# Kernel optimization log

Measured on AMD Instinct MI355X. Metric: run time of the kernel, lower is better.

Reference implementation:

```python
import jax, jax.numpy as jnp
import numpy as np
from functools import partial

INPUT_SIZE = 24
HIDDEN = 64
NUM_LAYERS = 3
OUT_FEATURES = 4


def _lstm_layer(x, w_ih, w_hh, b_ih, b_hh):
    """Single LSTM layer, PyTorch gate order (i, f, g, o).
    x: [B, T, in] -> returns h sequence [B, T, H]."""
    B = x.shape[0]
    H = w_hh.shape[1]
    # Precompute input contribution for all timesteps: [B, T, 4H]
    gx = jnp.einsum('bti,gi->btg', x, w_ih) + b_ih + b_hh

    def step(carry, g_t):
        h, c = carry
        gates = g_t + h @ w_hh.T  # [B, 4H]
        i, f, g, o = jnp.split(gates, 4, axis=-1)
        i = jax.nn.sigmoid(i)
        f = jax.nn.sigmoid(f)
        g = jnp.tanh(g)
        o = jax.nn.sigmoid(o)
        c = f * c + i * g
        h = o * jnp.tanh(c)
        return (h, c), h

    h0 = jnp.zeros((B, H), dtype=x.dtype)
    c0 = jnp.zeros((B, H), dtype=x.dtype)
    (_, _), hs = jax.lax.scan(step, (h0, c0), jnp.swapaxes(gx, 0, 1))  # hs: [T, B, H]
    return jnp.swapaxes(hs, 0, 1)  # [B, T, H]


def setup_inputs() -> dict:
    key = jax.random.key(0)
    ks = jax.random.split(key, 16)
    B, T = 1024, 512
    inp = {"x": jax.random.normal(ks[0], (B, T, INPUT_SIZE), dtype=jnp.float32)}
    k = 1
    s = 1.0 / np.sqrt(HIDDEN)
    for layer in range(NUM_LAYERS):
        in_dim = INPUT_SIZE if layer == 0 else HIDDEN
        inp[f"w_ih_{layer}"] = jax.random.uniform(ks[k], (4 * HIDDEN, in_dim), minval=-s, maxval=s, dtype=jnp.float32); k += 1
        inp[f"w_hh_{layer}"] = jax.random.uniform(ks[k], (4 * HIDDEN, HIDDEN), minval=-s, maxval=s, dtype=jnp.float32); k += 1
        inp[f"b_ih_{layer}"] = jax.random.uniform(ks[k], (4 * HIDDEN,), minval=-s, maxval=s, dtype=jnp.float32); k += 1
        inp[f"b_hh_{layer}"] = jax.random.uniform(ks[k], (4 * HIDDEN,), minval=-s, maxval=s, dtype=jnp.float32); k += 1
    inp["w_lin"] = jax.random.uniform(ks[13], (OUT_FEATURES, HIDDEN), minval=-s, maxval=s, dtype=jnp.float32)
    inp["b_lin"] = jax.random.uniform(ks[14], (OUT_FEATURES,), minval=-s, maxval=s, dtype=jnp.float32)
    return inp


def reference(x, w_ih_0, w_hh_0, b_ih_0, b_hh_0,
              w_ih_1, w_hh_1, b_ih_1, b_hh_1,
              w_ih_2, w_hh_2, b_ih_2, b_hh_2,
              w_lin, b_lin):
    params = [(w_ih_0, w_hh_0, b_ih_0, b_hh_0),
              (w_ih_1, w_hh_1, b_ih_1, b_hh_1),
              (w_ih_2, w_hh_2, b_ih_2, b_hh_2)]
    h = x
    for (w_ih, w_hh, b_ih, b_hh) in params:  # fixed 3-layer stack
        h = _lstm_layer(h, w_ih, w_hh, b_ih, b_hh)
    last = h[:, -1]                      # [B, H]
    return last @ w_lin.T + b_lin        # [B, 4]
```

## Files before the change

### kernel.cpp

```cpp
#include <hip/hip_runtime.h>


typedef __attribute__((ext_vector_type(8))) _Float16 half8;
typedef __attribute__((ext_vector_type(4))) float floatx4;

static constexpr int T_STEPS = 512;

#define NL2E  (-1.4426950408889634f)
#define N2L2E (-2.8853900817779268f)

#define H_OFF0   0
#define H_OFF1   1024
#define H_OFF2   2048
#define SM_BYTES 3072

__device__ __forceinline__ floatx4 mfma16(half8 a, half8 b, floatx4 c) {
    return __builtin_amdgcn_mfma_f32_16x16x32_f16(a, b, c, 0, 0, 0);
}

__device__ __forceinline__ half8 cvt8s(const float* src, float s) {
    float4 v0 = *(const float4*)(src);
    float4 v1 = *(const float4*)(src + 4);
    half8 h;
    h[0] = (_Float16)(v0.x * s); h[1] = (_Float16)(v0.y * s);
    h[2] = (_Float16)(v0.z * s); h[3] = (_Float16)(v0.w * s);
    h[4] = (_Float16)(v1.x * s); h[5] = (_Float16)(v1.y * s);
    h[6] = (_Float16)(v1.z * s); h[7] = (_Float16)(v1.w * s);
    return h;
}

__device__ __forceinline__ void lds_barrier() {
    asm volatile("s_waitcnt lgkmcnt(0)" ::: "memory");
    __builtin_amdgcn_s_barrier();
}

__global__ __launch_bounds__(768, 3) void lstm3_v10(
    const float* __restrict__ x,
    const float* __restrict__ w_ih0, const float* __restrict__ w_hh0,
    const float* __restrict__ b_ih0, const float* __restrict__ b_hh0,
    const float* __restrict__ w_ih1, const float* __restrict__ w_hh1,
    const float* __restrict__ b_ih1, const float* __restrict__ b_hh1,
    const float* __restrict__ w_ih2, const float* __restrict__ w_hh2,
    const float* __restrict__ b_ih2, const float* __restrict__ b_hh2,
    const float* __restrict__ w_lin, const float* __restrict__ b_lin,
    float* __restrict__ out)
{
    __shared__ __align__(16) char sm[SM_BYTES];

    const int tid  = threadIdx.x;
    const int lane = tid & 63;
    const int wave = tid >> 6;
    const int L    = wave >> 2;
    const int w    = wave & 3;
    const int l15  = lane & 15;
    const int l4   = lane >> 4;
    const int bat  = l15 >> 2;
    const int b0   = blockIdx.x * 4;
    const int u    = w * 16 + l15;

    for (int i = tid; i < SM_BYTES / 16; i += 768)
        *(floatx4*)(&sm[i * 16]) = floatx4{0.f, 0.f, 0.f, 0.f};

    const float* wi = (L == 0) ? w_ih0 : (L == 1 ? w_ih1 : w_ih2);
    const float* wh = (L == 0) ? w_hh0 : (L == 1 ? w_hh1 : w_hh2);
    const float* bi = (L == 0) ? b_ih0 : (L == 1 ? b_ih1 : b_ih2);
    const float* bh = (L == 0) ? b_hh0 : (L == 1 ? b_hh1 : b_hh2);
    const int HB = (L == 0) ? H_OFF0 : (L == 1 ? H_OFF1 : H_OFF2);
    const int PB = (L == 1) ? H_OFF0 : H_OFF1;

    half8 wf[4][4];
#pragma unroll
    for (int tt = 0; tt < 4; ++tt) {
        const int g = tt * 64 + u;
        const float sc = (tt == 2) ? N2L2E : NL2E;
        if (L == 0) {
            half8 z;
#pragma unroll
            for (int j = 0; j < 8; ++j) z[j] = (_Float16)0.f;
            wf[tt][0] = (l4 < 3) ? cvt8s(w_ih0 + g * 24 + l4 * 8, sc) : z;
            wf[tt][1] = cvt8s(w_hh0 + g * 64 + l4 * 8, sc);
            wf[tt][2] = cvt8s(w_hh0 + g * 64 + 32 + l4 * 8, sc);
            wf[tt][3] = z;
        } else {
            wf[tt][0] = cvt8s(wi + g * 64 + l4 * 8, sc);
            wf[tt][1] = cvt8s(wi + g * 64 + 32 + l4 * 8, sc);
            wf[tt][2] = cvt8s(wh + g * 64 + l4 * 8, sc);
            wf[tt][3] = cvt8s(wh + g * 64 + 32 + l4 * 8, sc);
        }
    }
    floatx4 bv[4];
#pragma unroll
    for (int tt = 0; tt < 4; ++tt) {
        const float sc = (tt == 2) ? N2L2E : NL2E;
        float b = sc * (bi[tt * 64 + u] + bh[tt * 64 + u]);
        bv[tt][0] = b; bv[tt][1] = b; bv[tt][2] = b; bv[tt][3] = b;
    }
    const floatx4 Z4 = floatx4{0.f, 0.f, 0.f, 0.f};

    const int swzR = (bat & 1) << 5;
    int rb0 = 0, rb1 = 0, rb2 = 0, rb3 = 0;
    if (L == 0) {
        rb1 = H_OFF0 + ((bat * 128 + 0  + l4 * 16) ^ swzR);
        rb2 = H_OFF0 + ((bat * 128 + 64 + l4 * 16) ^ swzR);
    } else {
        rb0 = PB + ((bat * 128 + 0  + l4 * 16) ^ swzR);
        rb1 = PB + ((bat * 128 + 64 + l4 * 16) ^ swzR);
        rb2 = HB + ((bat * 128 + 0  + l4 * 16) ^ swzR);
        rb3 = HB + ((bat * 128 + 64 + l4 * 16) ^ swzR);
    }
    const int wb = HB + ((l4 * 128 + u * 2) ^ ((l4 & 1) << 5));

    const int par_e = L & 1;
    const int so_e = par_e * 512, sp_e = (par_e ^ 1) * 512;
    const int eA0 = rb0 + so_e;
    const int eA1 = rb1 + ((L == 0) ? sp_e : so_e);
    const int eA2 = rb2 + sp_e;
    const int eA3 = rb3 + sp_e;
    const int eWr = wb + so_e;
    const int oA0 = rb0 + sp_e;
    const int oA1 = rb1 + ((L == 0) ? so_e : sp_e);
    const int oA2 = rb2 + so_e;
    const int oA3 = rb3 + so_e;
    const int oWr = wb + sp_e;

    float4 xA0{0,0,0,0}, xA1{0,0,0,0}, xB0{0,0,0,0}, xB1{0,0,0,0};
    const bool xv = (L == 0) && (l4 < 3);
    const float* xpe = nullptr;
    const float* xpo = nullptr;
    if (xv) {
        const float* xb_ = x + (long)(b0 + bat) * T_STEPS * 24 + l4 * 8;
        xA0 = *(const float4*)(xb_);      xA1 = *(const float4*)(xb_ + 4);
        xB0 = *(const float4*)(xb_ + 24); xB1 = *(const float4*)(xb_ + 28);
        xpe = xb_ + 48;
        xpo = xb_ + 72;
    }

    float cst = 0.0f;
    __syncthreads();

    auto body = [&](int s, int A0, int A1, int A2, int A3, int WR)
        __attribute__((always_inline)) {
        const int t = s - L;
        const bool active = ((unsigned)t < (unsigned)T_STEPS);

        if (active) {
            float pre0, pre1, pre2, pre3;
            __builtin_amdgcn_s_setprio(1);
            if (L == 0) {
                const float4 v0 = (t & 1) ? xB0 : xA0;
                const float4 v1 = (t & 1) ? xB1 : xA1;
                half8 aX;
                aX[0] = (_Float16)v0.x; aX[1] = (_Float16)v0.y;
                aX[2] = (_Float16)v0.z; aX[3] = (_Float16)v0.w;
                aX[4] = (_Float16)v1.x; aX[5] = (_Float16)v1.y;
                aX[6] = (_Float16)v1.z; aX[7] = (_Float16)v1.w;
                half8 a1 = *(const half8*)(&sm[A1]);
                half8 a2 = *(const half8*)(&sm[A2]);
#pragma unroll
                for (int tt = 0; tt < 4; ++tt) {
                    floatx4 accA = mfma16(aX, wf[tt][0], bv[tt]);
                    floatx4 accB = mfma16(a1, wf[tt][1], Z4);
                    accB = mfma16(a2, wf[tt][2], accB);
                    float p = accA[0] + accB[0];
                    if (tt == 0) pre0 = p; else if (tt == 1) pre1 = p;
                    else if (tt == 2) pre2 = p; else pre3 = p;
                }
                if (xv && t + 2 < T_STEPS) {
                    if (t & 1) {
                        xB0 = *(const float4*)(xpo); xB1 = *(const float4*)(xpo + 4);
                        xpo += 48;
                    } else {
                        xA0 = *(const float4*)(xpe); xA1 = *(const float4*)(xpe + 4);
                        xpe += 48;
                    }
                }
            } else {
                half8 a0 = *(const half8*)(&sm[A0]);
                half8 a1 = *(const half8*)(&sm[A1]);
                half8 a2 = *(const half8*)(&sm[A2]);
                half8 a3 = *(const half8*)(&sm[A3]);
#pragma unroll
                for (int tt = 0; tt < 4; ++tt) {
                    floatx4 accA = mfma16(a0, wf[tt][0], bv[tt]);
                    floatx4 accB = mfma16(a2, wf[tt][2], Z4);
                    accA = mfma16(a1, wf[tt][1], accA);
                    accB = mfma16(a3, wf[tt][3], accB);
                    float p = accA[0] + accB[0];
                    if (tt == 0) pre0 = p; else if (tt == 1) pre1 = p;
                    else if (tt == 2) pre2 = p; else pre3 = p;
                }
            }
            __builtin_amdgcn_s_setprio(0);

            float ei = __builtin_amdgcn_exp2f(pre0);
            float ef = __builtin_amdgcn_exp2f(pre1);
            float eg = __builtin_amdgcn_exp2f(pre2);
            float eo = __builtin_amdgcn_exp2f(pre3);
            float ig = __builtin_amdgcn_rcpf(1.f + ei);
            float fg = __builtin_amdgcn_rcpf(1.f + ef);
            float sg = __builtin_amdgcn_rcpf(1.f + eg);
            float og = __builtin_amdgcn_rcpf(1.f + eo);
            float gg = fmaf(2.f, sg, -1.f);
            cst = fmaf(fg, cst, ig * gg);
            float et = __builtin_amdgcn_exp2f(cst * N2L2E);
            float th = fmaf(2.f, __builtin_amdgcn_rcpf(1.f + et), -1.f);
            float hv = og * th;
            *(_Float16*)(&sm[WR]) = (_Float16)hv;
        }
        lds_barrier();
    };

    for (int s = 0; s < T_STEPS + 2; s += 2) {
        body(s,     eA0, eA1, eA2, eA3, eWr);
        body(s + 1, oA0, oA1, oA2, oA3, oWr);
    }

    __syncthreads();

    if (tid < 16) {
        const int bb = tid >> 2, o = tid & 3;
        const int sl = ((T_STEPS - 1) & 1) * 512;
        float accum = b_lin[o];
#pragma unroll
        for (int k = 0; k < 64; ++k) {
            const int off = H_OFF2 + sl + ((bb * 128 + k * 2) ^ ((bb & 1) << 5));
            accum = fmaf((float)*(const _Float16*)(&sm[off]), w_lin[o * 64 + k], accum);
        }
        out[(b0 + bb) * 4 + o] = accum;
    }
}

extern "C" void kernel_launch(void* const* d_in, const int* in_sizes, int n_in,
                              void* d_out, int out_size, void* d_ws, size_t ws_size,
                              hipStream_t stream) {
    const float* x     = (const float*)d_in[0];
    const float* w_ih0 = (const float*)d_in[1];
    const float* w_hh0 = (const float*)d_in[2];
    const float* b_ih0 = (const float*)d_in[3];
    const float* b_hh0 = (const float*)d_in[4];
    const float* w_ih1 = (const float*)d_in[5];
    const float* w_hh1 = (const float*)d_in[6];
    const float* b_ih1 = (const float*)d_in[7];
    const float* b_hh1 = (const float*)d_in[8];
    const float* w_ih2 = (const float*)d_in[9];
    const float* w_hh2 = (const float*)d_in[10];
    const float* b_ih2 = (const float*)d_in[11];
    const float* b_hh2 = (const float*)d_in[12];
    const float* w_lin = (const float*)d_in[13];
    const float* b_lin = (const float*)d_in[14];

    lstm3_v10<<<dim3(256), dim3(768), 0, stream>>>(
        x, w_ih0, w_hh0, b_ih0, b_hh0,
        w_ih1, w_hh1, b_ih1, b_hh1,
        w_ih2, w_hh2, b_ih2, b_hh2,
        w_lin, b_lin, (float*)d_out);
}
```

Baseline: 324.2 us.

## Stagger layer-2 waves by a half step to overlap MFMA with activations

Each recurrent step is split into two half-phases, each ending in an LDS barrier. Layers 0 and 1 run their MFMAs in the first half and their activations in the second, while layer 2 runs in the opposite order. Layer 2's matrix work therefore overlaps the other layers' transcendental work, and its h-buffer parity is flipped to match the shifted timeline. The cost is twice as many workgroup barriers per step and a few more loop iterations.

```diff
diff --git a/kernel.cpp b/kernel.cpp
--- a/kernel.cpp
+++ b/kernel.cpp
@@ -34,7 +34,7 @@
     __builtin_amdgcn_s_barrier();
 }
 
-__global__ __launch_bounds__(768, 3) void lstm3_v10(
+__global__ __launch_bounds__(768, 3) void lstm3_v11(
     const float* __restrict__ x,
     const float* __restrict__ w_ih0, const float* __restrict__ w_hh0,
     const float* __restrict__ b_ih0, const float* __restrict__ b_hh0,
@@ -116,12 +116,12 @@
     const int eA1 = rb1 + ((L == 0) ? sp_e : so_e);
     const int eA2 = rb2 + sp_e;
     const int eA3 = rb3 + sp_e;
-    const int eWr = wb + so_e;
+    const int eWr = wb + ((L == 2) ? sp_e : so_e);
     const int oA0 = rb0 + sp_e;
     const int oA1 = rb1 + ((L == 0) ? so_e : sp_e);
     const int oA2 = rb2 + so_e;
     const int oA3 = rb3 + so_e;
-    const int oWr = wb + sp_e;
+    const int oWr = wb + ((L == 2) ? so_e : sp_e);
 
     float4 xA0{0,0,0,0}, xA1{0,0,0,0}, xB0{0,0,0,0}, xB1{0,0,0,0};
     const bool xv = (L == 0) && (l4 < 3);
@@ -136,83 +136,99 @@
     }
 
     float cst = 0.0f;
+    float pre0 = 0.f, pre1 = 0.f, pre2 = 0.f, pre3 = 0.f;
     __syncthreads();
 
-    auto body = [&](int s, int A0, int A1, int A2, int A3, int WR)
+    auto do_mfma = [&](int t, int A0, int A1, int A2, int A3)
         __attribute__((always_inline)) {
-        const int t = s - L;
-        const bool active = ((unsigned)t < (unsigned)T_STEPS);
-
-        if (active) {
-            float pre0, pre1, pre2, pre3;
-            __builtin_amdgcn_s_setprio(1);
-            if (L == 0) {
-                const float4 v0 = (t & 1) ? xB0 : xA0;
-                const float4 v1 = (t & 1) ? xB1 : xA1;
-                half8 aX;
-                aX[0] = (_Float16)v0.x; aX[1] = (_Float16)v0.y;
-                aX[2] = (_Float16)v0.z; aX[3] = (_Float16)v0.w;
-                aX[4] = (_Float16)v1.x; aX[5] = (_Float16)v1.y;
-                aX[6] = (_Float16)v1.z; aX[7] = (_Float16)v1.w;
-                half8 a1 = *(const half8*)(&sm[A1]);
-                half8 a2 = *(const half8*)(&sm[A2]);
-#pragma unroll
-                for (int tt = 0; tt < 4; ++tt) {
-                    floatx4 accA = mfma16(aX, wf[tt][0], bv[tt]);
-                    floatx4 accB = mfma16(a1, wf[tt][1], Z4);
-                    accB = mfma16(a2, wf[tt][2], accB);
-                    float p = accA[0] + accB[0];
-                    if (tt == 0) pre0 = p; else if (tt == 1) pre1 = p;
-                    else if (tt == 2) pre2 = p; else pre3 = p;
-                }
-                if (xv && t + 2 < T_STEPS) {
-                    if (t & 1) {
-                        xB0 = *(const float4*)(xpo); xB1 = *(const float4*)(xpo + 4);
-                        xpo += 48;
-                    } else {
-                        xA0 = *(const float4*)(xpe); xA1 = *(const float4*)(xpe + 4);
-                        xpe += 48;
-                    }
-                }
-            } else {
-                half8 a0 = *(const half8*)(&sm[A0]);
-                half8 a1 = *(const half8*)(&sm[A1]);
-                half8 a2 = *(const half8*)(&sm[A2]);
-                half8 a3 = *(const half8*)(&sm[A3]);
-#pragma unroll
-                for (int tt = 0; tt < 4; ++tt) {
-                    floatx4 accA = mfma16(a0, wf[tt][0], bv[tt]);
-                    floatx4 accB = mfma16(a2, wf[tt][2], Z4);
-                    accA = mfma16(a1, wf[tt][1], accA);
-                    accB = mfma16(a3, wf[tt][3], accB);
-                    float p = accA[0] + accB[0];
-                    if (tt == 0) pre0 = p; else if (tt == 1) pre1 = p;
-                    else if (tt == 2) pre2 = p; else pre3 = p;
+        __builtin_amdgcn_s_setprio(1);
+        if (L == 0) {
+            const float4 v0 = (t & 1) ? xB0 : xA0;
+            const float4 v1 = (t & 1) ? xB1 : xA1;
+            half8 aX;
+            aX[0] = (_Float16)v0.x; aX[1] = (_Float16)v0.y;
+            aX[2] = (_Float16)v0.z; aX[3] = (_Float16)v0.w;
+            aX[4] = (_Float16)v1.x; aX[5] = (_Float16)v1.y;
+            aX[6] = (_Float16)v1.z; aX[7] = (_Float16)v1.w;
+            half8 a1 = *(const half8*)(&sm[A1]);
+            half8 a2 = *(const half8*)(&sm[A2]);
+#pragma unroll
+            for (int tt = 0; tt < 4; ++tt) {
+                floatx4 accA = mfma16(aX, wf[tt][0], bv[tt]);
+                floatx4 accB = mfma16(a1, wf[tt][1], Z4);
+                accB = mfma16(a2, wf[tt][2], accB);
+                float p = accA[0] + accB[0];
+                if (tt == 0) pre0 = p; else if (tt == 1) pre1 = p;
+                else if (tt == 2) pre2 = p; else pre3 = p;
+            }
+            if (xv && t + 2 < T_STEPS) {
+                if (t & 1) {
+                    xB0 = *(const float4*)(xpo); xB1 = *(const float4*)(xpo + 4);
+                    xpo += 48;
+                } else {
+                    xA0 = *(const float4*)(xpe); xA1 = *(const float4*)(xpe + 4);
+                    xpe += 48;
                 }
             }
-            __builtin_amdgcn_s_setprio(0);
-
-            float ei = __builtin_amdgcn_exp2f(pre0);
-            float ef = __builtin_amdgcn_exp2f(pre1);
-            float eg = __builtin_amdgcn_exp2f(pre2);
-            float eo = __builtin_amdgcn_exp2f(pre3);
-            float ig = __builtin_amdgcn_rcpf(1.f + ei);
-            float fg = __builtin_amdgcn_rcpf(1.f + ef);
-            float sg = __builtin_amdgcn_rcpf(1.f + eg);
-            float og = __builtin_amdgcn_rcpf(1.f + eo);
-            float gg = fmaf(2.f, sg, -1.f);
-            cst = fmaf(fg, cst, ig * gg);
-            float et = __builtin_amdgcn_exp2f(cst * N2L2E);
-            float th = fmaf(2.f, __builtin_amdgcn_rcpf(1.f + et), -1.f);
-            float hv = og * th;
-            *(_Float16*)(&sm[WR]) = (_Float16)hv;
+        } else {
+            half8 a0 = *(const half8*)(&sm[A0]);
+            half8 a1 = *(const half8*)(&sm[A1]);
+            half8 a2 = *(const half8*)(&sm[A2]);
+            half8 a3 = *(const half8*)(&sm[A3]);
+#pragma unroll
+            for (int tt = 0; tt < 4; ++tt) {
+                floatx4 accA = mfma16(a0, wf[tt][0], bv[tt]);
+                floatx4 accB = mfma16(a2, wf[tt][2], Z4);
+                accA = mfma16(a1, wf[tt][1], accA);
+                accB = mfma16(a3, wf[tt][3], accB);
+                float p = accA[0] + accB[0];
+                if (tt == 0) pre0 = p; else if (tt == 1) pre1 = p;
+                else if (tt == 2) pre2 = p; else pre3 = p;
+            }
+        }
+        __builtin_amdgcn_s_setprio(0);
+    };
+
+    auto do_act = [&](int WR) __attribute__((always_inline)) {
+        float ei = __builtin_amdgcn_exp2f(pre0);
+        float ef = __builtin_amdgcn_exp2f(pre1);
+        float eg = __builtin_amdgcn_exp2f(pre2);
+        float eo = __builtin_amdgcn_exp2f(pre3);
+        float ig = __builtin_amdgcn_rcpf(1.f + ei);
+        float fg = __builtin_amdgcn_rcpf(1.f + ef);
+        float sg = __builtin_amdgcn_rcpf(1.f + eg);
+        float og = __builtin_amdgcn_rcpf(1.f + eo);
+        float gg = fmaf(2.f, sg, -1.f);
+        cst = fmaf(fg, cst, ig * gg);
+        float et = __builtin_amdgcn_exp2f(cst * N2L2E);
+        float th = fmaf(2.f, __builtin_amdgcn_rcpf(1.f + et), -1.f);
+        float hv = og * th;
+        *(_Float16*)(&sm[WR]) = (_Float16)hv;
+    };
+
+    auto phase = [&](int k, int A0, int A1, int A2, int A3, int WR)
+        __attribute__((always_inline)) {
+        if (L < 2) {
+            const int t = k - L;
+            if ((unsigned)t < (unsigned)T_STEPS) do_mfma(t, A0, A1, A2, A3);
+        } else {
+            const int ta = k - 3;
+            if ((unsigned)ta < (unsigned)T_STEPS) do_act(WR);
+        }
+        lds_barrier();
+        if (L < 2) {
+            const int t = k - L;
+            if ((unsigned)t < (unsigned)T_STEPS) do_act(WR);
+        } else {
+            const int tm = k - 2;
+            if ((unsigned)tm < (unsigned)T_STEPS) do_mfma(tm, A0, A1, A2, A3);
         }
         lds_barrier();
     };
 
-    for (int s = 0; s < T_STEPS + 2; s += 2) {
-        body(s,     eA0, eA1, eA2, eA3, eWr);
-        body(s + 1, oA0, oA1, oA2, oA3, oWr);
+    for (int k = 0; k < T_STEPS + 4; k += 2) {
+        phase(k,     eA0, eA1, eA2, eA3, eWr);
+        phase(k + 1, oA0, oA1, oA2, oA3, oWr);
     }
 
     __syncthreads();
@@ -249,7 +265,7 @@
     const float* w_lin = (const float*)d_in[13];
     const float* b_lin = (const float*)d_in[14];
 
-    lstm3_v10<<<dim3(256), dim3(768), 0, stream>>>(
+    lstm3_v11<<<dim3(256), dim3(768), 0, stream>>>(
         x, w_ih0, w_hh0, b_ih0, b_hh0,
         w_ih1, w_hh1, b_ih1, b_hh1,
         w_ih2, w_hh2, b_ih2, b_hh2,
```

Measured after the change: 349.5 us. +7.8%, slower.
